# Optimization experiments

Measured on AMD Instinct MI355X. Metric: run time of the kernel, lower is better.

Reference implementation:

```python
import jax, jax.numpy as jnp
import numpy as np

L, H, D, DH, F = 2, 12, 768, 64, 3072
B, T = 2, 2048
LN_EPS = 1e-5


def setup_inputs() -> dict:
    key = jax.random.key(0)
    ks = jax.random.split(key, 16)
    s = 0.02
    inp = {
        "x": jax.random.normal(ks[0], (B, T, D), dtype=jnp.float32),
        "attn_mask": jnp.ones((1, T, T), dtype=jnp.int32),
        # per-layer, per-head QKV projections
        "Wq": jax.random.normal(ks[1], (L, H, D, DH), jnp.float32) * s,
        "bq": jnp.zeros((L, H, DH), jnp.float32),
        "Wk": jax.random.normal(ks[2], (L, H, D, DH), jnp.float32) * s,
        "bk": jnp.zeros((L, H, DH), jnp.float32),
        "Wv": jax.random.normal(ks[3], (L, H, D, DH), jnp.float32) * s,
        "bv": jnp.zeros((L, H, DH), jnp.float32),
        # output projection over concatenated heads
        "Wo": jax.random.normal(ks[4], (L, H * DH, D), jnp.float32) * s,
        "bo": jnp.zeros((L, D), jnp.float32),
        # FFN: LayerNorm -> Linear -> GELU -> Linear
        "ln_g": jnp.ones((L, D), jnp.float32),
        "ln_b": jnp.zeros((L, D), jnp.float32),
        "W1": jax.random.normal(ks[5], (L, D, F), jnp.float32) * s,
        "b1": jnp.zeros((L, F), jnp.float32),
        "W2": jax.random.normal(ks[6], (L, F, D), jnp.float32) * s,
        "b2": jnp.zeros((L, D), jnp.float32),
    }
    return inp


def _layer(x, mask, Wq, bq, Wk, bk, Wv, bv, Wo, bo, ln_g, ln_b, W1, b1, W2, b2):
    # batched multi-head attention (equivalent to per-head loop in source)
    q = jnp.einsum("btd,hde->bhte", x, Wq) + bq[None, :, None, :]
    k = jnp.einsum("btd,hde->bhte", x, Wk) + bk[None, :, None, :]
    v = jnp.einsum("btd,hde->bhte", x, Wv) + bv[None, :, None, :]
    scores = jnp.einsum("bhte,bhse->bhts", q, k) / np.sqrt(DH).astype(np.float32)
    scores = jnp.where(mask[:, None, :, :] == 0, -jnp.inf, scores)
    alpha = jax.nn.softmax(scores, axis=-1)
    attn = jnp.einsum("bhts,bhse->bhte", alpha, v)  # [B,H,T,DH]
    concat = attn.transpose(0, 2, 1, 3).reshape(x.shape[0], x.shape[1], H * DH)
    x = concat @ Wo + bo + x  # attention residual
    # FFN with pre-LayerNorm inside the block, residual around it
    mu = jnp.mean(x, axis=-1, keepdims=True)
    var = jnp.mean(jnp.square(x - mu), axis=-1, keepdims=True)
    h = (x - mu) * jax.lax.rsqrt(var + LN_EPS) * ln_g + ln_b
    h = jax.nn.gelu(h @ W1 + b1, approximate=False) @ W2 + b2
    return h + x


def reference(x, attn_mask, Wq, bq, Wk, bk, Wv, bv, Wo, bo, ln_g, ln_b, W1, b1, W2, b2):
    for l in range(L):
        x = _layer(x, attn_mask,
                   Wq[l], bq[l], Wk[l], bk[l], Wv[l], bv[l],
                   Wo[l], bo[l], ln_g[l], ln_b[l],
                   W1[l], b1[l], W2[l], b2[l])
    return x
```

## Files before the change

### kernel.cpp

```cpp
#include <hip/hip_runtime.h>
#include <math.h>

#define CL 2
#define CH 12
#define CD 768
#define CDH 64
#define CF 3072
#define CB 2
#define CT 2048
#define CBH (CB * CH)
#define CBTCD ((size_t)CB * CT * CD)

typedef __bf16 bf16x8 __attribute__((ext_vector_type(8)));
typedef float f32x4 __attribute__((ext_vector_type(4)));
typedef short s16x4 __attribute__((ext_vector_type(4)));
typedef ushort u16x4 __attribute__((ext_vector_type(4)));

#define QSCALE 0.18033688011112042f

__device__ __forceinline__ ushort f2bf(float f) {
  return __builtin_bit_cast(ushort, (__bf16)f);
}

__device__ __forceinline__ float fexp2(float x) {
  float r;
  asm volatile("v_exp_f32 %0, %1" : "=v"(r) : "v"(x));
  return r;
}

__device__ __forceinline__ float wred_sum(float v) {
#pragma unroll
  for (int o = 32; o > 0; o >>= 1) v += __shfl_xor(v, o);
  return v;
}

__device__ __forceinline__ void gload16(const ushort* g, ushort* l) {
  __builtin_amdgcn_global_load_lds(
      (const __attribute__((address_space(1))) unsigned int*)g,
      (__attribute__((address_space(3))) unsigned int*)l, 16, 0, 0);
}

enum { EPI_BF16 = 1, EPI_BIAS_BF16 = 2, EPI_BIAS_GELU_BF16 = 3, EPI_BIAS_RES_F32 = 4, EPI_BIAS_RES_F32_BF16 = 5, EPI_PART_F32 = 6, EPI_QKV = 7 };

template <int EPI>
__global__ __launch_bounds__(256) void gemm_k(
    const ushort* __restrict__ A, int lda,
    const ushort* __restrict__ B, int ldb,
    void* __restrict__ Cv, int ldc,
    int K,
    const float* __restrict__ bias,
    const float* __restrict__ res,
    ushort* __restrict__ C2) {
  __shared__ ushort As[3][128 * 32];
  __shared__ ushort Bs[3][128 * 32];
  const int tid = threadIdx.x;
  const int lane = tid & 63;
  const int wave = tid >> 6;
  const int wm = (wave >> 1) * 64;
  const int wn = (wave & 1) * 64;

  const int gx = gridDim.x;
  const int nwg = gx * gridDim.y;
  int wgid = blockIdx.y * gx + blockIdx.x;
  const int cpx = nwg >> 3;
  wgid = (wgid & 7) * cpx + (wgid >> 3);
  const int m0 = (wgid / gx) * 128;
  const int n0 = (wgid % gx) * 128;

  const int lr = lane & 15;
  const int lg = lane >> 4;
  f32x4 acc[4][4] = {};

  const int kz = blockIdx.z * K;
  const ushort* pa = A + (size_t)(m0 + (tid >> 2)) * lda + (tid & 3) * 8 + kz;
  const ushort* pb = B + (size_t)(n0 + (tid >> 2)) * ldb + (tid & 3) * 8 + kz;

  auto stage = [&](int buf, int k0) {
#pragma unroll
    for (int p = 0; p < 2; ++p) {
      gload16(pa + (size_t)p * 64 * lda + k0, &As[buf][wave * 512 + p * 2048]);
      gload16(pb + (size_t)p * 64 * ldb + k0, &Bs[buf][wave * 512 + p * 2048]);
    }
  };

  const int nt = K >> 5;
  stage(0, 0);
  stage(1, 32);
  for (int kt = 0; kt < nt; ++kt) {
    const int cur = kt % 3;
    if (kt + 2 < nt) {
      stage((kt + 2) % 3, (kt + 2) << 5);
      asm volatile("s_waitcnt vmcnt(8)" ::: "memory");
    } else if (kt + 1 < nt) {
      asm volatile("s_waitcnt vmcnt(4)" ::: "memory");
    } else {
      asm volatile("s_waitcnt vmcnt(0)" ::: "memory");
    }
    __builtin_amdgcn_s_barrier();
    __builtin_amdgcn_sched_barrier(0);

    bf16x8 af[4], bfr[4];
#pragma unroll
    for (int f = 0; f < 4; ++f) af[f] = *(const bf16x8*)(&As[cur][(wm + f * 16 + lr) * 32 + lg * 8]);
#pragma unroll
    for (int f = 0; f < 4; ++f) bfr[f] = *(const bf16x8*)(&Bs[cur][(wn + f * 16 + lr) * 32 + lg * 8]);
#pragma unroll
    for (int i = 0; i < 4; ++i)
#pragma unroll
      for (int j = 0; j < 4; ++j)
        acc[i][j] = __builtin_amdgcn_mfma_f32_16x16x32_bf16(af[i], bfr[j], acc[i][j], 0, 0, 0);

    __builtin_amdgcn_sched_barrier(0);
    __builtin_amdgcn_s_barrier();
  }

  const int cr0 = lg * 4;
#pragma unroll
  for (int i = 0; i < 4; ++i) {
#pragma unroll
    for (int j = 0; j < 4; ++j) {
      int col = n0 + wn + j * 16 + lr;
      if constexpr (EPI == EPI_QKV) {
        const int cbase = n0 + wn + j * 16;
        const int row0 = m0 + wm + i * 16 + cr0;
        float bcol = bias[col];
        if (cbase >= 2 * CD) {
          const int bb = row0 >> 11;
          const int t0 = row0 & (CT - 1);
          const int hh = (cbase - 2 * CD) >> 6;
          const int ee = ((cbase - 2 * CD) & 63) + lr;
          u16x4 o;
#pragma unroll
          for (int r = 0; r < 4; ++r) o[r] = f2bf(acc[i][j][r] + bcol);
          *(u16x4*)(C2 + ((size_t)(bb * CH + hh) * 64 + ee) * CT + t0) = o;
        } else {
#pragma unroll
          for (int r = 0; r < 4; ++r)
            ((ushort*)Cv)[(size_t)(row0 + r) * ldc + col] = f2bf(acc[i][j][r] + bcol);
        }
        continue;
      }
#pragma unroll
      for (int r = 0; r < 4; ++r) {
        int row = m0 + wm + i * 16 + cr0 + r;
        float val = acc[i][j][r];
        size_t offc = (size_t)row * ldc + col;
        if constexpr (EPI == EPI_BF16) {
          ((ushort*)Cv)[offc] = f2bf(val);
        } else if constexpr (EPI == EPI_BIAS_BF16) {
          ((ushort*)Cv)[offc] = f2bf(val + bias[col]);
        } else if constexpr (EPI == EPI_BIAS_GELU_BF16) {
          float x = val + bias[col];
          float gel = 0.5f * x * (1.0f + erff(x * 0.70710678118654752f));
          ((ushort*)Cv)[offc] = f2bf(gel);
        } else if constexpr (EPI == EPI_BIAS_RES_F32) {
          ((float*)Cv)[offc] = val + bias[col] + res[offc];
        } else if constexpr (EPI == EPI_PART_F32) {
          ((float*)Cv)[blockIdx.z * CBTCD + offc] = val;
        } else if constexpr (EPI == EPI_BIAS_RES_F32_BF16) {
          float o = val + bias[col] + res[offc];
          ((float*)Cv)[offc] = o;
          C2[offc] = f2bf(o);
        }
      }
    }
  }
}

template <bool DUAL>
__global__ __launch_bounds__(256) void reduce2_k(const float* __restrict__ part,
                                                 const float* __restrict__ bias,
                                                 const float* __restrict__ res,
                                                 float* __restrict__ outf,
                                                 ushort* __restrict__ outb) {
  int i = blockIdx.x * 256 + threadIdx.x;
  float4 p0 = ((const float4*)part)[i];
  float4 p1 = ((const float4*)(part + CBTCD))[i];
  float4 rr = ((const float4*)res)[i];
  int col = (i * 4) % CD;
  float4 bb = *(const float4*)(bias + col);
  float4 o;
  o.x = p0.x + p1.x + rr.x + bb.x;
  o.y = p0.y + p1.y + rr.y + bb.y;
  o.z = p0.z + p1.z + rr.z + bb.z;
  o.w = p0.w + p1.w + rr.w + bb.w;
  ((float4*)outf)[i] = o;
  if constexpr (DUAL) {
    ushort4 u;
    u.x = f2bf(o.x); u.y = f2bf(o.y); u.z = f2bf(o.z); u.w = f2bf(o.w);
    ((ushort4*)outb)[i] = u;
  }
}

__global__ __launch_bounds__(256) void flash_k(const ushort* __restrict__ qkv,
                                               const ushort* __restrict__ vt,
                                               const unsigned* __restrict__ mbits,
                                               ushort* __restrict__ out) {
  const int q0 = blockIdx.x * 64;
  const int bh = blockIdx.y;
  const int b = bh / CH, h = bh % CH;
  const int tid = threadIdx.x;
  const int lane = tid & 63;
  const int wave = tid >> 6;
  const int lr = lane & 15;
  const int lg = lane >> 4;

  __shared__ ushort Ks[2][64][72];
  __shared__ ushort Vt[2][64][72];

  const int qg = q0 + wave * 16 + lr;
  const ushort* qrow = qkv + ((size_t)(b * CT) + qg) * 2304 + h * CDH;
  bf16x8 aq0 = *(const bf16x8*)(qrow + lg * 8);
  bf16x8 aq1 = *(const bf16x8*)(qrow + 32 + lg * 8);

  f32x4 acc[4] = {};
  float m_run = -1e30f, l_run = 0.f;

  const ushort* kbase = qkv + (size_t)(b * CT) * 2304 + CD + h * CDH;
  const ushort* vbase = vt + (size_t)bh * 64 * CT;

  const int r0 = tid >> 3, r1 = 32 + (tid >> 3), cc = (tid & 7) * 8;

  auto ld = [&](int kv0, bf16x8& k0, bf16x8& k1, bf16x8& v0, bf16x8& v1) {
    k0 = *(const bf16x8*)(kbase + (size_t)(kv0 + r0) * 2304 + cc);
    k1 = *(const bf16x8*)(kbase + (size_t)(kv0 + r1) * 2304 + cc);
    v0 = *(const bf16x8*)(vbase + (size_t)r0 * CT + kv0 + cc);
    v1 = *(const bf16x8*)(vbase + (size_t)r1 * CT + kv0 + cc);
  };
  auto st = [&](int buf, bf16x8 k0, bf16x8 k1, bf16x8 v0, bf16x8 v1) {
    *(bf16x8*)(&Ks[buf][r0][cc]) = k0;
    *(bf16x8*)(&Ks[buf][r1][cc]) = k1;
    *(bf16x8*)(&Vt[buf][r0][cc]) = v0;
    *(bf16x8*)(&Vt[buf][r1][cc]) = v1;
  };
  auto bar = [&]() {
    asm volatile("s_waitcnt lgkmcnt(0)" ::: "memory");
    __builtin_amdgcn_s_barrier();
    __builtin_amdgcn_sched_barrier(0);
  };

  auto compute = [&](int kv0, int buf) {
    f32x4 stt[4];
    __builtin_amdgcn_s_setprio(1);
#pragma unroll
    for (int j = 0; j < 4; ++j) {
      bf16x8 kf0 = *(const bf16x8*)(&Ks[buf][j * 16 + lr][lg * 8]);
      bf16x8 kf1 = *(const bf16x8*)(&Ks[buf][j * 16 + lr][32 + lg * 8]);
      f32x4 t = {};
      t = __builtin_amdgcn_mfma_f32_16x16x32_bf16(kf0, aq0, t, 0, 0, 0);
      t = __builtin_amdgcn_mfma_f32_16x16x32_bf16(kf1, aq1, t, 0, 0, 0);
      stt[j] = t;
    }
    __builtin_amdgcn_s_setprio(0);

    unsigned w0 = mbits[(size_t)qg * 64 + (kv0 >> 5)];
    unsigned w1 = mbits[(size_t)qg * 64 + (kv0 >> 5) + 1];
    float tmax = -INFINITY;
    if ((w0 & w1) == 0xFFFFFFFFu) {
#pragma unroll
      for (int j = 0; j < 4; ++j)
#pragma unroll
        for (int r = 0; r < 4; ++r) tmax = fmaxf(tmax, stt[j][r]);
    } else {
#pragma unroll
      for (int j = 0; j < 4; ++j) {
        unsigned w = (j < 2) ? w0 : w1;
#pragma unroll
        for (int r = 0; r < 4; ++r) {
          int bit = (j * 16 + lg * 4 + r) & 31;
          if (((w >> bit) & 1u) == 0u) stt[j][r] = -INFINITY;
          tmax = fmaxf(tmax, stt[j][r]);
        }
      }
    }
    tmax = fmaxf(tmax, __shfl_xor(tmax, 16));
    tmax = fmaxf(tmax, __shfl_xor(tmax, 32));

    if (__any(tmax - m_run > 8.0f)) {
      float mnew = fmaxf(m_run, tmax);
      float sc = fexp2(m_run - mnew);
      m_run = mnew;
      l_run *= sc;
#pragma unroll
      for (int jj = 0; jj < 4; ++jj) {
        acc[jj][0] *= sc; acc[jj][1] *= sc; acc[jj][2] *= sc; acc[jj][3] *= sc;
      }
    }

    s16x4 pf[4];
#pragma unroll
    for (int j = 0; j < 4; ++j) {
      s16x4 pv;
#pragma unroll
      for (int r = 0; r < 4; ++r) {
        float p = fexp2(stt[j][r] - m_run);
        l_run += p;
        pv[r] = (short)f2bf(p);
      }
      pf[j] = pv;
    }

    __builtin_amdgcn_s_setprio(1);
#pragma unroll
    for (int jj = 0; jj < 4; ++jj) {
#pragma unroll
      for (int j = 0; j < 4; ++j) {
        s16x4 vf = *(const s16x4*)(&Vt[buf][jj * 16 + lr][j * 16 + lg * 4]);
        acc[jj] = __builtin_amdgcn_mfma_f32_16x16x16bf16_1k(vf, pf[j], acc[jj], 0, 0, 0);
      }
    }
    __builtin_amdgcn_s_setprio(0);
  };

  bf16x8 kx0, kx1, vx0, vx1, ky0, ky1, vy0, vy1;
  ld(0, kx0, kx1, vx0, vx1);
  ld(64, ky0, ky1, vy0, vy1);
  st(0, kx0, kx1, vx0, vx1);
  bar();
  for (int t = 0; t < 32; t += 2) {
    if (t + 2 < 32) ld((t + 2) * 64, kx0, kx1, vx0, vx1);
    compute(t * 64, 0);
    st(1, ky0, ky1, vy0, vy1);
    bar();
    if (t + 3 < 32) ld((t + 3) * 64, ky0, ky1, vy0, vy1);
    compute((t + 1) * 64, 1);
    if (t + 2 < 32) {
      st(0, kx0, kx1, vx0, vx1);
      bar();
    }
  }

  l_run += __shfl_xor(l_run, 16);
  l_run += __shfl_xor(l_run, 32);

  float inv = 1.0f / l_run;
  const int orow = b * CT + qg;
#pragma unroll
  for (int jj = 0; jj < 4; ++jj) {
    u16x4 o;
#pragma unroll
    for (int r = 0; r < 4; ++r) o[r] = f2bf(acc[jj][r] * inv);
    *(u16x4*)(out + (size_t)orow * CD + h * CDH + jj * 16 + lg * 4) = o;
  }
}

__global__ void maskbits_k(const int* __restrict__ mask, unsigned* __restrict__ mbits) {
  int idx = blockIdx.x * 256 + threadIdx.x;
  if (idx >= CT * 64) return;
  const int* mp = mask + (size_t)(idx >> 6) * CT + (idx & 63) * 32;
  unsigned bits = 0;
#pragma unroll
  for (int j = 0; j < 32; ++j) bits |= (mp[j] != 0 ? 1u : 0u) << j;
  mbits[idx] = bits;
}

__global__ __launch_bounds__(256) void ln_k(const float* __restrict__ X,
                                            ushort* __restrict__ H,
                                            const float* __restrict__ g,
                                            const float* __restrict__ b) {
  const int t = blockIdx.x;
  const int tid = threadIdx.x;
  const float* row = X + (size_t)t * CD;
  float x0 = row[tid], x1 = row[tid + 256], x2 = row[tid + 512];
  float s = wred_sum(x0 + x1 + x2);
  __shared__ float sh[4], sh2[4];
  if ((tid & 63) == 0) sh[tid >> 6] = s;
  __syncthreads();
  float mu = (sh[0] + sh[1] + sh[2] + sh[3]) * (1.0f / 768.0f);
  float d0 = x0 - mu, d1 = x1 - mu, d2 = x2 - mu;
  float vs = wred_sum(d0 * d0 + d1 * d1 + d2 * d2);
  if ((tid & 63) == 0) sh2[tid >> 6] = vs;
  __syncthreads();
  float var = (sh2[0] + sh2[1] + sh2[2] + sh2[3]) * (1.0f / 768.0f);
  float r = 1.0f / sqrtf(var + 1e-5f);
  H[(size_t)t * CD + tid] = f2bf(d0 * r * g[tid] + b[tid]);
  H[(size_t)t * CD + tid + 256] = f2bf(d1 * r * g[tid + 256] + b[tid + 256]);
  H[(size_t)t * CD + tid + 512] = f2bf(d2 * r * g[tid + 512] + b[tid + 512]);
}

__global__ void f32_to_bf16_k(const float* __restrict__ in, ushort* __restrict__ out, int n4) {
  int i = blockIdx.x * 256 + threadIdx.x;
  if (i >= n4) return;
  float4 f = *(const float4*)(in + (size_t)i * 4);
  ushort4 u;
  u.x = f2bf(f.x); u.y = f2bf(f.y); u.z = f2bf(f.z); u.w = f2bf(f.w);
  *(ushort4*)(out + (size_t)i * 4) = u;
}

__global__ __launch_bounds__(256) void tcvt_k(const float* __restrict__ src, size_t sbs,
                                              ushort* __restrict__ dst, size_t dbs,
                                              int R, int C, float scale) {
  __shared__ float t[32][33];
  const float* s = src + blockIdx.z * sbs;
  ushort* d = dst + blockIdx.z * dbs;
  const int tx = threadIdx.x & 31;
  const int ty4 = (threadIdx.x >> 5) * 4;
  const int r0 = blockIdx.y * 32, c0 = blockIdx.x * 32;
#pragma unroll
  for (int i = 0; i < 4; ++i) t[ty4 + i][tx] = s[(size_t)(r0 + ty4 + i) * C + c0 + tx];
  __syncthreads();
#pragma unroll
  for (int i = 0; i < 4; ++i)
    d[(size_t)(c0 + ty4 + i) * R + r0 + tx] = f2bf(t[tx][ty4 + i] * scale);
}

__global__ void repack_bqkv_k(const float* __restrict__ bq, const float* __restrict__ bk,
                              const float* __restrict__ bv, float* __restrict__ dst) {
  int idx = blockIdx.x * 256 + threadIdx.x;
  if (idx >= CL * 2304) return;
  int l = idx / 2304;
  int c = idx % 2304;
  int sec = c / CD;
  int within = c % CD;
  int h = within / CDH;
  int e = within % CDH;
  const float* B = (sec == 0) ? bq : ((sec == 1) ? bk : bv);
  float v = B[((size_t)l * CH + h) * CDH + e];
  if (sec == 0) v *= QSCALE;
  dst[idx] = v;
}

extern "C" void kernel_launch(void* const* d_in, const int* in_sizes, int n_in,
                              void* d_out, int out_size, void* d_ws, size_t ws_size,
                              hipStream_t stream) {
  (void)in_sizes; (void)n_in; (void)out_size; (void)ws_size;
  const float* X = (const float*)d_in[0];
  const int* MSK = (const int*)d_in[1];
  const float* Wq = (const float*)d_in[2];
  const float* bq = (const float*)d_in[3];
  const float* Wk = (const float*)d_in[4];
  const float* bk = (const float*)d_in[5];
  const float* Wv = (const float*)d_in[6];
  const float* bv = (const float*)d_in[7];
  const float* Wo = (const float*)d_in[8];
  const float* bo = (const float*)d_in[9];
  const float* lng = (const float*)d_in[10];
  const float* lnb = (const float*)d_in[11];
  const float* W1 = (const float*)d_in[12];
  const float* b1 = (const float*)d_in[13];
  const float* W2 = (const float*)d_in[14];
  const float* b2 = (const float*)d_in[15];

  char* base = (char*)d_ws;
  size_t off = 0;
  auto alloc = [&](size_t bytes) {
    char* p = base + off;
    off = (off + bytes + 255) & ~(size_t)255;
    return p;
  };
  ushort* wqkv_t = (ushort*)alloc((size_t)CL * 2304 * CD * 2);
  ushort* wo_t = (ushort*)alloc((size_t)CL * CD * CD * 2);
  ushort* w1_t = (ushort*)alloc((size_t)CL * CF * CD * 2);
  ushort* w2_t = (ushort*)alloc((size_t)CL * CD * CF * 2);
  float* bqkv = (float*)alloc((size_t)CL * 2304 * 4);
  ushort* xb = (ushort*)alloc((size_t)CB * CT * CD * 2);
  ushort* qkv = (ushort*)alloc((size_t)CB * CT * 2304 * 2);
  ushort* vt = (ushort*)alloc((size_t)CB * CH * CDH * CT * 2);
  unsigned* mbits = (unsigned*)alloc((size_t)CT * 64 * 4);
  ushort* attno = (ushort*)alloc((size_t)CB * CT * CD * 2);
  float* xattn = (float*)alloc((size_t)CB * CT * CD * 4);
  float* xf = (float*)alloc((size_t)CB * CT * CD * 4);
  ushort* hln = (ushort*)alloc((size_t)CB * CT * CD * 2);
  ushort* gbuf = (ushort*)alloc((size_t)CB * CT * CF * 2);
  float* part = (float*)qkv;

  const int BT_ = CB * CT;

  for (int l = 0; l < CL; ++l) {
    tcvt_k<<<dim3(CDH / 32, CD / 32, CH), 256, 0, stream>>>(
        Wq + (size_t)l * CH * CD * CDH, (size_t)CD * CDH,
        wqkv_t + (size_t)l * 2304 * CD + 0 * CD * CD, (size_t)CDH * CD,
        CD, CDH, QSCALE);
    tcvt_k<<<dim3(CDH / 32, CD / 32, CH), 256, 0, stream>>>(
        Wk + (size_t)l * CH * CD * CDH, (size_t)CD * CDH,
        wqkv_t + (size_t)l * 2304 * CD + 1 * CD * CD, (size_t)CDH * CD,
        CD, CDH, 1.0f);
    tcvt_k<<<dim3(CDH / 32, CD / 32, CH), 256, 0, stream>>>(
        Wv + (size_t)l * CH * CD * CDH, (size_t)CD * CDH,
        wqkv_t + (size_t)l * 2304 * CD + 2 * CD * CD, (size_t)CDH * CD,
        CD, CDH, 1.0f);
  }
  tcvt_k<<<dim3(CD / 32, CD / 32, CL), 256, 0, stream>>>(
      Wo, (size_t)CD * CD, wo_t, (size_t)CD * CD, CD, CD, 1.0f);
  tcvt_k<<<dim3(CF / 32, CD / 32, CL), 256, 0, stream>>>(
      W1, (size_t)CD * CF, w1_t, (size_t)CF * CD, CD, CF, 1.0f);
  tcvt_k<<<dim3(CD / 32, CF / 32, CL), 256, 0, stream>>>(
      W2, (size_t)CF * CD, w2_t, (size_t)CD * CF, CF, CD, 1.0f);
  {
    int n = CL * 2304;
    repack_bqkv_k<<<(n + 255) / 256, 256, 0, stream>>>(bq, bk, bv, bqkv);
  }
  maskbits_k<<<(CT * 64 + 255) / 256, 256, 0, stream>>>(MSK, mbits);

  {
    int n4 = BT_ * CD / 4;
    f32_to_bf16_k<<<(n4 + 255) / 256, 256, 0, stream>>>(X, xb, n4);
  }

  for (int l = 0; l < CL; ++l) {
    const float* xcur = (l == 0) ? X : xf;
    gemm_k<EPI_QKV><<<dim3(2304 / 128, BT_ / 128), 256, 0, stream>>>(
        xb, CD, wqkv_t + (size_t)l * 2304 * CD, CD, qkv, 2304, CD,
        bqkv + (size_t)l * 2304, nullptr, vt);
    flash_k<<<dim3(CT / 64, CBH), 256, 0, stream>>>(qkv, vt, mbits, attno);
    gemm_k<EPI_BIAS_RES_F32><<<dim3(CD / 128, BT_ / 128), 256, 0, stream>>>(
        attno, CD, wo_t + (size_t)l * CD * CD, CD, xattn, CD, CD,
        bo + (size_t)l * CD, xcur, nullptr);
    ln_k<<<BT_, 256, 0, stream>>>(xattn, hln, lng + (size_t)l * CD, lnb + (size_t)l * CD);
    gemm_k<EPI_BIAS_GELU_BF16><<<dim3(CF / 128, BT_ / 128), 256, 0, stream>>>(
        hln, CD, w1_t + (size_t)l * CF * CD, CD, gbuf, CF, CD,
        b1 + (size_t)l * CF, nullptr, nullptr);
    gemm_k<EPI_PART_F32><<<dim3(CD / 128, BT_ / 128, 2), 256, 0, stream>>>(
        gbuf, CF, w2_t + (size_t)l * CD * CF, CF, part, CD, CF / 2,
        nullptr, nullptr, nullptr);
    const int nred = BT_ * CD / 4 / 256;
    if (l == CL - 1) {
      reduce2_k<false><<<nred, 256, 0, stream>>>(part, b2 + (size_t)l * CD, xattn,
                                                 (float*)d_out, nullptr);
    } else {
      reduce2_k<true><<<nred, 256, 0, stream>>>(part, b2 + (size_t)l * CD, xattn,
                                                xf, xb);
    }
  }
}
```

Baseline: 431.4 us.

## Swizzle flash K/V shared tiles and precompute per-row all-ones mask flag

```diff
diff --git a/kernel.cpp b/kernel.cpp
--- a/kernel.cpp
+++ b/kernel.cpp
@@ -195,6 +195,7 @@
 __global__ __launch_bounds__(256) void flash_k(const ushort* __restrict__ qkv,
                                                const ushort* __restrict__ vt,
                                                const unsigned* __restrict__ mbits,
+                                               const unsigned char* __restrict__ rowall,
                                                ushort* __restrict__ out) {
   const int q0 = blockIdx.x * 64;
   const int bh = blockIdx.y;
@@ -205,8 +206,8 @@
   const int lr = lane & 15;
   const int lg = lane >> 4;
 
-  __shared__ ushort Ks[2][64][72];
-  __shared__ ushort Vt[2][64][72];
+  __shared__ ushort Ks[2][64 * 64];
+  __shared__ ushort Vt[2][64 * 64];
 
   const int qg = q0 + wave * 16 + lr;
   const ushort* qrow = qkv + ((size_t)(b * CT) + qg) * 2304 + h * CDH;
@@ -215,11 +216,20 @@
 
   f32x4 acc[4] = {};
   float m_run = -1e30f, l_run = 0.f;
+  const bool am = rowall[qg] != 0;
 
   const ushort* kbase = qkv + (size_t)(b * CT) * 2304 + CD + h * CDH;
   const ushort* vbase = vt + (size_t)bh * 64 * CT;
 
   const int r0 = tid >> 3, r1 = 32 + (tid >> 3), cc = (tid & 7) * 8;
+  const int ssl = (((tid & 7) ^ (r0 & 7)) * 8);
+
+  const int koff0 = ((lg ^ (lr & 7)) * 8);
+  const int koff1 = (((4 + lg) ^ (lr & 7)) * 8);
+  int voff[4];
+#pragma unroll
+  for (int j = 0; j < 4; ++j)
+    voff[j] = (((2 * j + (lg >> 1)) ^ (lr & 7)) * 8) + (lg & 1) * 4;
 
   auto ld = [&](int kv0, bf16x8& k0, bf16x8& k1, bf16x8& v0, bf16x8& v1) {
     k0 = *(const bf16x8*)(kbase + (size_t)(kv0 + r0) * 2304 + cc);
@@ -228,10 +238,10 @@
     v1 = *(const bf16x8*)(vbase + (size_t)r1 * CT + kv0 + cc);
   };
   auto st = [&](int buf, bf16x8 k0, bf16x8 k1, bf16x8 v0, bf16x8 v1) {
-    *(bf16x8*)(&Ks[buf][r0][cc]) = k0;
-    *(bf16x8*)(&Ks[buf][r1][cc]) = k1;
-    *(bf16x8*)(&Vt[buf][r0][cc]) = v0;
-    *(bf16x8*)(&Vt[buf][r1][cc]) = v1;
+    *(bf16x8*)(&Ks[buf][r0 * 64 + ssl]) = k0;
+    *(bf16x8*)(&Ks[buf][r1 * 64 + ssl]) = k1;
+    *(bf16x8*)(&Vt[buf][r0 * 64 + ssl]) = v0;
+    *(bf16x8*)(&Vt[buf][r1 * 64 + ssl]) = v1;
   };
   auto bar = [&]() {
     asm volatile("s_waitcnt lgkmcnt(0)" ::: "memory");
@@ -244,8 +254,8 @@
     __builtin_amdgcn_s_setprio(1);
 #pragma unroll
     for (int j = 0; j < 4; ++j) {
-      bf16x8 kf0 = *(const bf16x8*)(&Ks[buf][j * 16 + lr][lg * 8]);
-      bf16x8 kf1 = *(const bf16x8*)(&Ks[buf][j * 16 + lr][32 + lg * 8]);
+      bf16x8 kf0 = *(const bf16x8*)(&Ks[buf][(j * 16 + lr) * 64 + koff0]);
+      bf16x8 kf1 = *(const bf16x8*)(&Ks[buf][(j * 16 + lr) * 64 + koff1]);
       f32x4 t = {};
       t = __builtin_amdgcn_mfma_f32_16x16x32_bf16(kf0, aq0, t, 0, 0, 0);
       t = __builtin_amdgcn_mfma_f32_16x16x32_bf16(kf1, aq1, t, 0, 0, 0);
@@ -253,15 +263,15 @@
     }
     __builtin_amdgcn_s_setprio(0);
 
-    unsigned w0 = mbits[(size_t)qg * 64 + (kv0 >> 5)];
-    unsigned w1 = mbits[(size_t)qg * 64 + (kv0 >> 5) + 1];
     float tmax = -INFINITY;
-    if ((w0 & w1) == 0xFFFFFFFFu) {
+    if (am) {
 #pragma unroll
       for (int j = 0; j < 4; ++j)
 #pragma unroll
         for (int r = 0; r < 4; ++r) tmax = fmaxf(tmax, stt[j][r]);
     } else {
+      unsigned w0 = mbits[(size_t)qg * 64 + (kv0 >> 5)];
+      unsigned w1 = mbits[(size_t)qg * 64 + (kv0 >> 5) + 1];
 #pragma unroll
       for (int j = 0; j < 4; ++j) {
         unsigned w = (j < 2) ? w0 : w1;
@@ -305,7 +315,7 @@
     for (int jj = 0; jj < 4; ++jj) {
 #pragma unroll
       for (int j = 0; j < 4; ++j) {
-        s16x4 vf = *(const s16x4*)(&Vt[buf][jj * 16 + lr][j * 16 + lg * 4]);
+        s16x4 vf = *(const s16x4*)(&Vt[buf][(jj * 16 + lr) * 64 + voff[j]]);
         acc[jj] = __builtin_amdgcn_mfma_f32_16x16x16bf16_1k(vf, pf[j], acc[jj], 0, 0, 0);
       }
     }
@@ -352,6 +362,16 @@
 #pragma unroll
   for (int j = 0; j < 32; ++j) bits |= (mp[j] != 0 ? 1u : 0u) << j;
   mbits[idx] = bits;
+}
+
+__global__ void rowall_k(const unsigned* __restrict__ mbits,
+                         unsigned char* __restrict__ rowall) {
+  int t = blockIdx.x * 256 + threadIdx.x;
+  if (t >= CT) return;
+  unsigned a = 0xFFFFFFFFu;
+#pragma unroll 8
+  for (int j = 0; j < 64; ++j) a &= mbits[(size_t)t * 64 + j];
+  rowall[t] = (a == 0xFFFFFFFFu) ? 1 : 0;
 }
 
 __global__ __launch_bounds__(256) void ln_k(const float* __restrict__ X,
@@ -457,6 +477,7 @@
   ushort* qkv = (ushort*)alloc((size_t)CB * CT * 2304 * 2);
   ushort* vt = (ushort*)alloc((size_t)CB * CH * CDH * CT * 2);
   unsigned* mbits = (unsigned*)alloc((size_t)CT * 64 * 4);
+  unsigned char* rowall = (unsigned char*)alloc((size_t)CT);
   ushort* attno = (ushort*)alloc((size_t)CB * CT * CD * 2);
   float* xattn = (float*)alloc((size_t)CB * CT * CD * 4);
   float* xf = (float*)alloc((size_t)CB * CT * CD * 4);
@@ -491,6 +512,7 @@
     repack_bqkv_k<<<(n + 255) / 256, 256, 0, stream>>>(bq, bk, bv, bqkv);
   }
   maskbits_k<<<(CT * 64 + 255) / 256, 256, 0, stream>>>(MSK, mbits);
+  rowall_k<<<(CT + 255) / 256, 256, 0, stream>>>(mbits, rowall);
 
   {
     int n4 = BT_ * CD / 4;
@@ -502,7 +524,7 @@
     gemm_k<EPI_QKV><<<dim3(2304 / 128, BT_ / 128), 256, 0, stream>>>(
         xb, CD, wqkv_t + (size_t)l * 2304 * CD, CD, qkv, 2304, CD,
         bqkv + (size_t)l * 2304, nullptr, vt);
-    flash_k<<<dim3(CT / 64, CBH), 256, 0, stream>>>(qkv, vt, mbits, attno);
+    flash_k<<<dim3(CT / 64, CBH), 256, 0, stream>>>(qkv, vt, mbits, rowall, attno);
     gemm_k<EPI_BIAS_RES_F32><<<dim3(CD / 128, BT_ / 128), 256, 0, stream>>>(
         attno, CD, wo_t + (size_t)l * CD * CD, CD, xattn, CD, CD,
         bo + (size_t)l * CD, xcur, nullptr);
```

After: 424.9 us. Within noise of the previous version (-1.5%).
